# Kernel optimization log

Hardware: AMD Instinct MI355X
Metric: run time of the kernel (lower is better)

## Reference

```python
import jax, jax.numpy as jnp
import numpy as np


def setup_inputs() -> dict:
    key = jax.random.key(0)
    ks = jax.random.split(key, 4)
    B, T, C = 2, 4096, 512
    x = jax.random.normal(ks[0], (B, T, C), dtype=jnp.float32)
    Wqkv = jax.random.normal(ks[1], (C, 3 * C), dtype=jnp.float32) * (C ** -0.5)
    bqkv = jnp.zeros((3 * C,), dtype=jnp.float32)
    Wout = jax.random.normal(ks[2], (C, C), dtype=jnp.float32) * (C ** -0.5)
    bout = jnp.zeros((C,), dtype=jnp.float32)
    return {"x": x, "Wqkv": Wqkv, "bqkv": bqkv, "Wout": Wout, "bout": bout}


def reference(x, Wqkv, bqkv, Wout, bout):
    B, T, C = x.shape
    H = 8
    D = C // H  # head_dim
    qkv = x @ Wqkv + bqkv                       # [B, T, 3C]
    qkv = qkv.reshape(B, T, 3, H, D)
    q, k, v = qkv[:, :, 0], qkv[:, :, 1], qkv[:, :, 2]  # [B, T, H, D]
    scale = 1.0 / np.sqrt(D).astype(np.float32)
    scores = jnp.einsum("bqhd,bkhd->bhqk", q, k) * scale  # [B, H, T, T]
    causal = jnp.tril(jnp.ones((T, T), dtype=bool))
    scores = jnp.where(causal, scores, jnp.finfo(scores.dtype).min)
    attn = jax.nn.softmax(scores, axis=-1)                 # [B, H, T, T]
    out = jnp.einsum("bhqk,bkhd->bqhd", attn, v).reshape(B, T, C)
    return out @ Wout + bout
```

## Files before the change

kernel.cpp:

```cpp
#include <hip/hip_runtime.h>
#include <hip/hip_bf16.h>
#include <cstdint>
#include <cstddef>

typedef __attribute__((ext_vector_type(8))) __bf16 bf16x8;
typedef __attribute__((ext_vector_type(4))) float f32x4;
typedef __attribute__((ext_vector_type(16))) float f32x16;

__device__ __forceinline__ ushort f2b(float x) {
    union { float f; uint32_t u; } v; v.f = x;
    uint32_t r = v.u + 0x7FFFu + ((v.u >> 16) & 1u);
    return (ushort)(r >> 16);
}

__device__ __forceinline__ void glds16(const void* g, void* l) {
    __builtin_amdgcn_global_load_lds(
        (const __attribute__((address_space(1))) void*)g,
        (__attribute__((address_space(3))) void*)l, 16, 0, 0);
}

__device__ __forceinline__ uint32_t cvt_pk_bf16(float lo, float hi) {
    uint32_t r;
    asm("v_cvt_pk_bf16_f32 %0, %1, %2" : "=v"(r) : "v"(lo), "v"(hi));
    return r;
}

__device__ __forceinline__ void plane_swap(uint32_t& a, uint32_t& b) {
    asm volatile("v_permlane32_swap_b32 %0, %1" : "+v"(a), "+v"(b));
}

__device__ __forceinline__ f32x16 z16() {
    f32x16 v;
#pragma unroll
    for (int i = 0; i < 16; ++i) v[i] = 0.f;
    return v;
}

__global__ __launch_bounds__(256) void k_prep(const float* __restrict__ x,
                                              ushort* __restrict__ xb,
                                              const float* __restrict__ Wqkv,
                                              ushort* __restrict__ wqkvT,
                                              const float* __restrict__ Wout,
                                              ushort* __restrict__ woutT) {
    __shared__ float tile[32][33];
    const int id = blockIdx.x;
    const int tid = threadIdx.x;
    if (id < 2048) {
        const int i = id * 256 + tid;
        const float4* p = (const float4*)x + (size_t)i * 2;
        float4 a = p[0], b = p[1];
        ushort o[8] = { f2b(a.x), f2b(a.y), f2b(a.z), f2b(a.w),
                        f2b(b.x), f2b(b.y), f2b(b.z), f2b(b.w) };
        *(uint4*)(xb + (size_t)i * 8) = *(const uint4*)o;
        return;
    }
    const float* in;
    ushort* out;
    int R = 512, C, c0, r0;
    if (id < 2816) {
        in = Wqkv; out = wqkvT; C = 1536;
        c0 = ((id - 2048) % 48) * 32; r0 = ((id - 2048) / 48) * 32;
    } else {
        in = Wout; out = woutT; C = 512;
        c0 = ((id - 2816) % 16) * 32; r0 = ((id - 2816) / 16) * 32;
    }
    const int tx = tid & 31, ty = tid >> 5;
#pragma unroll
    for (int i = 0; i < 32; i += 8)
        tile[ty + i][tx] = in[(size_t)(r0 + ty + i) * C + c0 + tx];
    __syncthreads();
#pragma unroll
    for (int i = 0; i < 32; i += 8)
        out[(size_t)(c0 + ty + i) * R + r0 + tx] = f2b(tile[tx][ty + i]);
}

template <int MODE, int MP>
__global__ __launch_bounds__(256) void k_gemm(const ushort* __restrict__ A,
                                              const ushort* __restrict__ BT,
                                              const float* __restrict__ bias,
                                              float* __restrict__ outF,
                                              ushort* __restrict__ Qp,
                                              ushort* __restrict__ Kp,
                                              ushort* __restrict__ VTp,
                                              int K) {
    __shared__ __align__(16) ushort lA[2][MP * 1024];
    __shared__ __align__(16) ushort lB[2][4096];
    const int tid = threadIdx.x;
    const int lane = tid & 63, lr = lane & 15, lg = lane >> 4;
    const int wid = tid >> 6, wm = wid >> 1, wn = wid & 1;
    const int m0 = blockIdx.x * (32 * MP), n0 = blockIdx.y * 128;

    const ushort* ga = A + (size_t)(m0 + (tid >> 2)) * K + (tid & 3) * 8;
    const ushort* gb = BT + (size_t)(n0 + (tid >> 2)) * K + (tid & 3) * 8;
    const size_t rstep = (size_t)64 * K;

    float bvv[4];
#pragma unroll
    for (int n = 0; n < 4; ++n) bvv[n] = bias[n0 + wn * 64 + n * 16 + lr];
    asm volatile("s_waitcnt vmcnt(0)" ::: "memory");
    __builtin_amdgcn_sched_barrier(0);

    f32x4 zero = {0.f, 0.f, 0.f, 0.f};
    f32x4 acc[MP][4];
#pragma unroll
    for (int i = 0; i < MP; ++i)
#pragma unroll
        for (int j = 0; j < 4; ++j) acc[i][j] = zero;

    auto STG = [&](int buf, int k0) {
        glds16(ga + k0, &lA[buf][tid * 8]);
        if constexpr (MP == 4) glds16(ga + k0 + rstep, &lA[buf][2048 + tid * 8]);
        glds16(gb + k0,         &lB[buf][tid * 8]);
        glds16(gb + k0 + rstep, &lB[buf][2048 + tid * 8]);
    };

    const int NT = K >> 5;
    STG(0, 0);
    for (int it = 0; it < NT; ++it) {
        const int bsel = it & 1;
        if (it + 1 < NT) {
            STG(bsel ^ 1, (it + 1) * 32);
            if constexpr (MP == 4) {
                asm volatile("s_waitcnt vmcnt(4)" ::: "memory");
            } else {
                asm volatile("s_waitcnt vmcnt(3)" ::: "memory");
            }
        } else {
            asm volatile("s_waitcnt vmcnt(0)" ::: "memory");
        }
        __builtin_amdgcn_sched_barrier(0);
        __builtin_amdgcn_s_barrier();
        asm volatile("" ::: "memory");

        bf16x8 af[MP], bfr[4];
#pragma unroll
        for (int m = 0; m < MP; ++m)
            af[m] = *(const bf16x8*)&lA[bsel][(wm * (16 * MP) + m * 16 + lr) * 32 + lg * 8];
#pragma unroll
        for (int n = 0; n < 4; ++n)
            bfr[n] = *(const bf16x8*)&lB[bsel][(wn * 64 + n * 16 + lr) * 32 + lg * 8];
#pragma unroll
        for (int m = 0; m < MP; ++m)
#pragma unroll
            for (int n = 0; n < 4; ++n)
                acc[m][n] = __builtin_amdgcn_mfma_f32_16x16x32_bf16(af[m], bfr[n], acc[m][n], 0, 0, 0);

        asm volatile("" ::: "memory");
        __builtin_amdgcn_s_barrier();
    }

#pragma unroll
    for (int n = 0; n < 4; ++n) {
        const int gn = n0 + wn * 64 + n * 16 + lr;
        const float bv = bvv[n];
#pragma unroll
        for (int m = 0; m < MP; ++m) {
            const int gmb = m0 + wm * (16 * MP) + m * 16 + lg * 4;
            if (MODE == 0) {
                const int sec = gn >> 9, c = gn & 511;
                const int h = c >> 6, d = c & 63;
                const int b = gmb >> 12, t = gmb & 4095;
                if (sec == 2) {
                    ushort tmp[4];
#pragma unroll
                    for (int r = 0; r < 4; ++r) tmp[r] = f2b(acc[m][n][r] + bv);
                    *(ushort4*)&VTp[(size_t)(b * 8 + h) * 262144 + (size_t)d * 4096 + t] =
                        *(const ushort4*)tmp;
                } else {
                    const size_t idx0 = ((size_t)(b * 8 + h) * 4096 + t) * 64 + d;
#pragma unroll
                    for (int r = 0; r < 4; ++r) {
                        const float v = acc[m][n][r] + bv;
                        if (sec == 0) Qp[idx0 + (size_t)r * 64] = f2b(v * 0.18033688f);
                        else          Kp[idx0 + (size_t)r * 64] = f2b(v);
                    }
                }
            } else {
#pragma unroll
                for (int r = 0; r < 4; ++r)
                    outF[(size_t)(gmb + r) * 512 + gn] = acc[m][n][r] + bv;
            }
        }
    }
}

template <int MODE>
__device__ __forceinline__ void attn_run(const ushort* __restrict__ Qb,
                                         const ushort* __restrict__ Kb,
                                         const ushort* __restrict__ Vb,
                                         ushort* sm, int qt, int kv_lo, int kv_hi,
                                         int lane, int w, int tid,
                                         ushort* __restrict__ Outp, int bh,
                                         float* __restrict__ pO,
                                         float* __restrict__ pL) {
    const int lg2 = lane >> 5, l31 = lane & 31, l7 = lane & 7;
    const int q0 = qt * 256;
    const int qbase = q0 + w * 32;

    bf16x8 qf[4];
#pragma unroll
    for (int ks = 0; ks < 4; ++ks)
        qf[ks] = *(const bf16x8*)&Qb[(size_t)(qbase + l31) * 64 + ks * 16 + lg2 * 8];
    asm volatile("s_waitcnt vmcnt(0)" ::: "memory");
    __builtin_amdgcn_sched_barrier(0);

    const int srow = tid >> 3;
    const int sslot = (tid & 7) ^ (srow & 7);

    auto STAGE = [&](int buf, int kv0) {
        glds16(Kb + (size_t)(kv0 + srow) * 64 + sslot * 8,
               (char*)sm + buf * 16384 + w * 1024);
        glds16(Vb + (size_t)srow * 4096 + kv0 + sslot * 8,
               (char*)sm + buf * 16384 + 8192 + w * 1024);
    };

    f32x16 oacc0 = z16(), oacc1 = z16();
    float lrun = 0.f;

    STAGE(0, kv_lo * 64);
    for (int it = kv_lo; it < kv_hi; ++it) {
        const int kv0 = it * 64;
        const int bsel = (it - kv_lo) & 1;
        if (it + 1 < kv_hi) {
            STAGE(bsel ^ 1, kv0 + 64);
            asm volatile("s_waitcnt vmcnt(2)" ::: "memory");
        } else {
            asm volatile("s_waitcnt vmcnt(0)" ::: "memory");
        }
        __builtin_amdgcn_sched_barrier(0);
        __builtin_amdgcn_s_barrier();
        asm volatile("" ::: "memory");

        const bool live0 = (kv0 <= qbase + 31);
        const bool live1 = (kv0 + 32 <= qbase + 31);
        if (live0) {
            const ushort* bK = sm + bsel * 8192;
            const ushort* bV = bK + 4096;

            f32x16 st0 = z16(), st1 = z16();
            __builtin_amdgcn_s_setprio(1);
#pragma unroll
            for (int ks = 0; ks < 4; ++ks) {
                bf16x8 kf = *(const bf16x8*)&bK[l31 * 64 + (((2 * ks + lg2) ^ l7)) * 8];
                st0 = __builtin_amdgcn_mfma_f32_32x32x16_bf16(kf, qf[ks], st0, 0, 0, 0);
            }
            if (live1) {
#pragma unroll
                for (int ks = 0; ks < 4; ++ks) {
                    bf16x8 kf = *(const bf16x8*)&bK[(32 + l31) * 64 + (((2 * ks + lg2) ^ l7)) * 8];
                    st1 = __builtin_amdgcn_mfma_f32_32x32x16_bf16(kf, qf[ks], st1, 0, 0, 0);
                }
            }
            __builtin_amdgcn_s_setprio(0);
            if (kv0 == qbase) {
#pragma unroll
                for (int r = 0; r < 16; ++r) {
                    const int rowk = (r & 3) + 8 * (r >> 2) + 4 * lg2;
                    if (rowk > l31) st0[r] = -1e30f;
                }
            }
            if (live1 && kv0 + 32 == qbase) {
#pragma unroll
                for (int r = 0; r < 16; ++r) {
                    const int rowk = (r & 3) + 8 * (r >> 2) + 4 * lg2;
                    if (rowk > l31) st1[r] = -1e30f;
                }
            }

            float s0 = 0.f, s1 = 0.f, s2 = 0.f, s3 = 0.f;
#pragma unroll
            for (int r = 0; r < 16; r += 4) {
                st0[r]     = __builtin_amdgcn_exp2f(st0[r]);     s0 += st0[r];
                st0[r + 1] = __builtin_amdgcn_exp2f(st0[r + 1]); s1 += st0[r + 1];
                st0[r + 2] = __builtin_amdgcn_exp2f(st0[r + 2]); s2 += st0[r + 2];
                st0[r + 3] = __builtin_amdgcn_exp2f(st0[r + 3]); s3 += st0[r + 3];
            }
            if (live1) {
#pragma unroll
                for (int r = 0; r < 16; r += 4) {
                    st1[r]     = __builtin_amdgcn_exp2f(st1[r]);     s0 += st1[r];
                    st1[r + 1] = __builtin_amdgcn_exp2f(st1[r + 1]); s1 += st1[r + 1];
                    st1[r + 2] = __builtin_amdgcn_exp2f(st1[r + 2]); s2 += st1[r + 2];
                    st1[r + 3] = __builtin_amdgcn_exp2f(st1[r + 3]); s3 += st1[r + 3];
                }
            }
            lrun += (s0 + s1) + (s2 + s3);

#pragma unroll
            for (int stp = 0; stp < 4; ++stp) {
                if (stp >= 2 && !live1) continue;
                const int h = stp & 1;
                uint32_t a0, a1, b0, b1;
                if (stp < 2) {
                    a0 = cvt_pk_bf16(st0[h * 8 + 0], st0[h * 8 + 1]);
                    a1 = cvt_pk_bf16(st0[h * 8 + 2], st0[h * 8 + 3]);
                    b0 = cvt_pk_bf16(st0[h * 8 + 4], st0[h * 8 + 5]);
                    b1 = cvt_pk_bf16(st0[h * 8 + 6], st0[h * 8 + 7]);
                } else {
                    a0 = cvt_pk_bf16(st1[h * 8 + 0], st1[h * 8 + 1]);
                    a1 = cvt_pk_bf16(st1[h * 8 + 2], st1[h * 8 + 3]);
                    b0 = cvt_pk_bf16(st1[h * 8 + 4], st1[h * 8 + 5]);
                    b1 = cvt_pk_bf16(st1[h * 8 + 6], st1[h * 8 + 7]);
                }
                plane_swap(a0, b0);
                plane_swap(a1, b1);
                union { uint32_t u[4]; bf16x8 v; } pk;
                pk.u[0] = a0; pk.u[1] = a1; pk.u[2] = b0; pk.u[3] = b1;
                const int vs = (((2 * stp + lg2) ^ l7)) * 8;
                bf16x8 vf0 = *(const bf16x8*)&bV[l31 * 64 + vs];
                bf16x8 vf1 = *(const bf16x8*)&bV[(32 + l31) * 64 + vs];
                __builtin_amdgcn_s_setprio(1);
                oacc0 = __builtin_amdgcn_mfma_f32_32x32x16_bf16(vf0, pk.v, oacc0, 0, 0, 0);
                oacc1 = __builtin_amdgcn_mfma_f32_32x32x16_bf16(vf1, pk.v, oacc1, 0, 0, 0);
                __builtin_amdgcn_s_setprio(0);
            }
        }
        asm volatile("" ::: "memory");
        __builtin_amdgcn_s_barrier();
    }

    lrun += __shfl_xor(lrun, 32);

    if (MODE == 0) {
        const float inv = 1.0f / lrun;
        ushort* ep = sm + w * 2304;
#pragma unroll
        for (int r = 0; r < 16; ++r) {
            const int dd = (r & 3) + 8 * (r >> 2) + 4 * lg2;
            ep[l31 * 72 + dd]      = f2b(oacc0[r] * inv);
            ep[l31 * 72 + 32 + dd] = f2b(oacc1[r] * inv);
        }
        asm volatile("s_waitcnt lgkmcnt(0)" ::: "memory");
        __builtin_amdgcn_sched_barrier(0);
        const int qq = lane >> 1, half = lane & 1;
        const int bb = bh >> 3, hh = bh & 7;
        const int tg = q0 + w * 32 + qq;
        ushort* op = Outp + ((size_t)(bb * 4096 + tg) * 512 + hh * 64 + half * 32);
#pragma unroll
        for (int j = 0; j < 4; ++j) {
            uint4 v = *(const uint4*)&ep[qq * 72 + half * 32 + j * 8];
            *(uint4*)&op[j * 8] = v;
        }
    } else {
        const int qc = w * 32 + l31;
#pragma unroll
        for (int r = 0; r < 16; ++r) {
            const int dd = (r & 3) + 8 * (r >> 2) + 4 * lg2;
            pO[dd * 256 + qc]        = oacc0[r];
            pO[(dd + 32) * 256 + qc] = oacc1[r];
        }
        if (lg2 == 0) pL[qc] = lrun;
    }
}

__global__ __launch_bounds__(512) void k_attn(const ushort* __restrict__ Q,
                                              const ushort* __restrict__ K,
                                              const ushort* __restrict__ VT,
                                              ushort* __restrict__ Outp,
                                              float* __restrict__ pO,
                                              float* __restrict__ pL) {
    __shared__ __align__(16) ushort sm[20480];
    const int tid = threadIdx.x;
    const int lane = tid & 63, w = tid >> 6;
    const int bh = blockIdx.x;
    const int s = blockIdx.y;
    const int p = s >> 1, half = s & 1;
    const int qtH = 15 - p;
    const size_t base = (size_t)bh * 4096 * 64;
    const ushort* Qb = Q + base;
    const ushort* Kb = K + base;
    const ushort* Vb = VT + base;

    const size_t slot = (size_t)(bh * 8 + p) * 2 + half;
    if (half == 0) {
        attn_run<1>(Qb, Kb, Vb, sm, qtH, 0, 34, lane, w, tid, nullptr, bh,
                    pO + slot * 16384, pL + slot * 256);
    } else {
        attn_run<1>(Qb, Kb, Vb, sm, qtH, 34, 64 - 4 * p, lane, w, tid, nullptr, bh,
                    pO + slot * 16384, pL + slot * 256);
        attn_run<0>(Qb, Kb, Vb, sm, p, 0, 4 * p + 4, lane, w, tid, Outp, bh,
                    nullptr, nullptr);
    }
}

__global__ __launch_bounds__(512) void k_merge(const float* __restrict__ pO,
                                               const float* __restrict__ pL,
                                               ushort* __restrict__ Outp) {
    const int bh = blockIdx.x;
    const int p = blockIdx.y;
    const int tid = threadIdx.x;
    const int q = tid >> 1, dh = (tid & 1) * 32;
    const size_t slot = (size_t)(bh * 8 + p) * 2;
    const float* OA = pO + slot * 16384;
    const float* OB = OA + 16384;
    const float la = pL[slot * 256 + q];
    const float lb = pL[slot * 256 + 256 + q];
    const float inv = 1.0f / (la + lb);
    ushort outv[32];
#pragma unroll
    for (int j = 0; j < 32; ++j) {
        const float o = (OA[(dh + j) * 256 + q] + OB[(dh + j) * 256 + q]) * inv;
        outv[j] = f2b(o);
    }
    const int b = bh >> 3, h = bh & 7;
    const int t = (15 - p) * 256 + q;
    ushort* op = Outp + ((size_t)(b * 4096 + t) * 512 + h * 64 + dh);
#pragma unroll
    for (int j = 0; j < 4; ++j) *(uint4*)&op[j * 8] = *(const uint4*)&outv[j * 8];
}

extern "C" void kernel_launch(void* const* d_in, const int* in_sizes, int n_in,
                              void* d_out, int out_size, void* d_ws, size_t ws_size,
                              hipStream_t stream) {
    const float* x    = (const float*)d_in[0];
    const float* Wqkv = (const float*)d_in[1];
    const float* bqkv = (const float*)d_in[2];
    const float* Wout = (const float*)d_in[3];
    const float* bout = (const float*)d_in[4];
    float* out = (float*)d_out;

    char* ws = (char*)d_ws;
    ushort* xb    = (ushort*)(ws);
    ushort* wqkvT = (ushort*)(ws + 8388608);
    ushort* woutT = (ushort*)(ws + 9961472);
    ushort* Qp    = (ushort*)(ws + 10485760);
    ushort* Kp    = (ushort*)(ws + 18874368);
    ushort* VTp   = (ushort*)(ws + 27262976);
    float*  pO    = (float*)(ws + 35651584);
    float*  pL    = (float*)(ws + 52428800);

    k_prep<<<3072, 256, 0, stream>>>(x, xb, Wqkv, wqkvT, Wout, woutT);
    k_gemm<0, 4><<<dim3(64, 12), 256, 0, stream>>>(xb, wqkvT, bqkv, nullptr, Qp, Kp, VTp, 512);
    k_attn<<<dim3(16, 16), 512, 0, stream>>>(Qp, Kp, VTp, xb, pO, pL);
    k_merge<<<dim3(16, 8), 512, 0, stream>>>(pO, pL, xb);
    k_gemm<1, 2><<<dim3(128, 4), 256, 0, stream>>>(xb, woutT, bout, out, nullptr, nullptr, nullptr, 512);
}
```

Before: 102.8 us.

## Split attention KV ranges into finer chunks and merge bf16 partials for all tiles

The causal attention work is repartitioned. Each high/low query-tile pair is now split across four blocks of 17 KV tiles, so the grid doubles from 256 to 512 blocks and the per-block load is more even. Every block now writes unnormalized partial outputs in bf16 plus row sums. A generalized merge kernel combines 1 to 4 partials per query tile. Partial buffers are placed in reused workspace and in the output buffer. This is meant to fill the CUs better and shrink the tail of the attention kernel, at the cost of more merge traffic and extra bf16 rounding of the unnormalized partials.

Measured after the change: 97.07 us (median of 2 runs). -5.5%, faster.

```diff
diff --git a/kernel.cpp b/kernel.cpp
--- a/kernel.cpp
+++ b/kernel.cpp
@@ -11,6 +11,11 @@
     union { float f; uint32_t u; } v; v.f = x;
     uint32_t r = v.u + 0x7FFFu + ((v.u >> 16) & 1u);
     return (ushort)(r >> 16);
+}
+
+__device__ __forceinline__ float b2f(ushort u) {
+    union { uint32_t u; float f; } v; v.u = (uint32_t)u << 16;
+    return v.f;
 }
 
 __device__ __forceinline__ void glds16(const void* g, void* l) {
@@ -184,14 +189,12 @@
     }
 }
 
-template <int MODE>
 __device__ __forceinline__ void attn_run(const ushort* __restrict__ Qb,
                                          const ushort* __restrict__ Kb,
                                          const ushort* __restrict__ Vb,
                                          ushort* sm, int qt, int kv_lo, int kv_hi,
                                          int lane, int w, int tid,
-                                         ushort* __restrict__ Outp, int bh,
-                                         float* __restrict__ pO,
+                                         ushort* __restrict__ pOb,
                                          float* __restrict__ pL) {
     const int lg2 = lane >> 5, l31 = lane & 31, l7 = lane & 7;
     const int q0 = qt * 256;
@@ -320,90 +323,100 @@
     }
 
     lrun += __shfl_xor(lrun, 32);
-
-    if (MODE == 0) {
-        const float inv = 1.0f / lrun;
-        ushort* ep = sm + w * 2304;
-#pragma unroll
-        for (int r = 0; r < 16; ++r) {
-            const int dd = (r & 3) + 8 * (r >> 2) + 4 * lg2;
-            ep[l31 * 72 + dd]      = f2b(oacc0[r] * inv);
-            ep[l31 * 72 + 32 + dd] = f2b(oacc1[r] * inv);
-        }
-        asm volatile("s_waitcnt lgkmcnt(0)" ::: "memory");
-        __builtin_amdgcn_sched_barrier(0);
-        const int qq = lane >> 1, half = lane & 1;
-        const int bb = bh >> 3, hh = bh & 7;
-        const int tg = q0 + w * 32 + qq;
-        ushort* op = Outp + ((size_t)(bb * 4096 + tg) * 512 + hh * 64 + half * 32);
-#pragma unroll
-        for (int j = 0; j < 4; ++j) {
-            uint4 v = *(const uint4*)&ep[qq * 72 + half * 32 + j * 8];
-            *(uint4*)&op[j * 8] = v;
-        }
-    } else {
-        const int qc = w * 32 + l31;
-#pragma unroll
-        for (int r = 0; r < 16; ++r) {
-            const int dd = (r & 3) + 8 * (r >> 2) + 4 * lg2;
-            pO[dd * 256 + qc]        = oacc0[r];
-            pO[(dd + 32) * 256 + qc] = oacc1[r];
-        }
-        if (lg2 == 0) pL[qc] = lrun;
-    }
+    const int qc = w * 32 + l31;
+#pragma unroll
+    for (int r = 0; r < 16; ++r) {
+        const int dd = (r & 3) + 8 * (r >> 2) + 4 * lg2;
+        pOb[dd * 256 + qc]        = f2b(oacc0[r]);
+        pOb[(dd + 32) * 256 + qc] = f2b(oacc1[r]);
+    }
+    if (lg2 == 0) pL[qc] = lrun;
 }
 
 __global__ __launch_bounds__(512) void k_attn(const ushort* __restrict__ Q,
                                               const ushort* __restrict__ K,
                                               const ushort* __restrict__ VT,
-                                              ushort* __restrict__ Outp,
-                                              float* __restrict__ pO,
+                                              ushort* __restrict__ hOb,
+                                              ushort* __restrict__ lOb,
                                               float* __restrict__ pL) {
-    __shared__ __align__(16) ushort sm[20480];
+    __shared__ __align__(16) ushort sm[16384];
     const int tid = threadIdx.x;
     const int lane = tid & 63, w = tid >> 6;
     const int bh = blockIdx.x;
     const int s = blockIdx.y;
-    const int p = s >> 1, half = s & 1;
-    const int qtH = 15 - p;
+    const int p = s >> 2, half = (s >> 1) & 1, sub = s & 1;
     const size_t base = (size_t)bh * 4096 * 64;
     const ushort* Qb = Q + base;
     const ushort* Kb = K + base;
     const ushort* Vb = VT + base;
 
-    const size_t slot = (size_t)(bh * 8 + p) * 2 + half;
+    const int pairbase = bh * 8 + p;
     if (half == 0) {
-        attn_run<1>(Qb, Kb, Vb, sm, qtH, 0, 34, lane, w, tid, nullptr, bh,
-                    pO + slot * 16384, pL + slot * 256);
+        const size_t hs = (size_t)(pairbase * 4 + sub);
+        attn_run(Qb, Kb, Vb, sm, 15 - p, 17 * sub, 17 * sub + 17, lane, w, tid,
+                 hOb + hs * 16384, pL + hs * 256);
     } else {
-        attn_run<1>(Qb, Kb, Vb, sm, qtH, 34, 64 - 4 * p, lane, w, tid, nullptr, bh,
-                    pO + slot * 16384, pL + slot * 256);
-        attn_run<0>(Qb, Kb, Vb, sm, p, 0, 4 * p + 4, lane, w, tid, Outp, bh,
-                    nullptr, nullptr);
-    }
-}
-
-__global__ __launch_bounds__(512) void k_merge(const float* __restrict__ pO,
+        const int nH2 = 30 - 4 * p;
+        if (17 * sub < nH2) {
+            const int hi = 17 * sub + 17 < nH2 ? 17 * sub + 17 : nH2;
+            const size_t hs = (size_t)(pairbase * 4 + 2 + sub);
+            attn_run(Qb, Kb, Vb, sm, 15 - p, 34 + 17 * sub, 34 + hi, lane, w, tid,
+                     hOb + hs * 16384, pL + hs * 256);
+        }
+        if (17 * sub + 17 > nH2) {
+            const int nL = 4 * p + 4;
+            int llo = 17 * sub - nH2; if (llo < 0) llo = 0;
+            int lhi = 17 * sub + 17 - nH2; if (lhi > nL) lhi = nL;
+            const int lidx = (p <= 3) ? 0 : sub;
+            const size_t ls = (size_t)(pairbase * 2 + lidx);
+            attn_run(Qb, Kb, Vb, sm, p, llo, lhi, lane, w, tid,
+                     lOb + ls * 16384, pL + (size_t)(512 + ls) * 256);
+        }
+    }
+}
+
+__global__ __launch_bounds__(512) void k_merge(const ushort* __restrict__ hOb,
+                                               const ushort* __restrict__ lOb,
                                                const float* __restrict__ pL,
                                                ushort* __restrict__ Outp) {
     const int bh = blockIdx.x;
-    const int p = blockIdx.y;
+    const int qt = blockIdx.y;
     const int tid = threadIdx.x;
     const int q = tid >> 1, dh = (tid & 1) * 32;
-    const size_t slot = (size_t)(bh * 8 + p) * 2;
-    const float* OA = pO + slot * 16384;
-    const float* OB = OA + 16384;
-    const float la = pL[slot * 256 + q];
-    const float lb = pL[slot * 256 + 256 + q];
-    const float inv = 1.0f / (la + lb);
+
+    int k;
+    const ushort* Ob;
+    const float* Lb;
+    if (qt >= 8) {
+        const int p = 15 - qt;
+        k = (p <= 3) ? 4 : 3;
+        const size_t s0 = (size_t)((bh * 8 + p) * 4);
+        Ob = hOb + s0 * 16384;
+        Lb = pL + s0 * 256;
+    } else {
+        const int p = qt;
+        k = (p <= 3) ? 1 : 2;
+        const size_t s0 = (size_t)((bh * 8 + p) * 2);
+        Ob = lOb + s0 * 16384;
+        Lb = pL + (size_t)(512 + s0) * 256;
+    }
+
+    float osum[32];
+#pragma unroll
+    for (int e = 0; e < 32; ++e) osum[e] = 0.f;
+    float lsum = 0.f;
+    for (int j = 0; j < k; ++j) {
+        const ushort* O = Ob + (size_t)j * 16384;
+#pragma unroll
+        for (int e = 0; e < 32; ++e) osum[e] += b2f(O[(dh + e) * 256 + q]);
+        lsum += Lb[(size_t)j * 256 + q];
+    }
+    const float inv = 1.0f / lsum;
     ushort outv[32];
 #pragma unroll
-    for (int j = 0; j < 32; ++j) {
-        const float o = (OA[(dh + j) * 256 + q] + OB[(dh + j) * 256 + q]) * inv;
-        outv[j] = f2b(o);
-    }
+    for (int e = 0; e < 32; ++e) outv[e] = f2b(osum[e] * inv);
     const int b = bh >> 3, h = bh & 7;
-    const int t = (15 - p) * 256 + q;
+    const int t = qt * 256 + q;
     ushort* op = Outp + ((size_t)(b * 4096 + t) * 512 + h * 64 + dh);
 #pragma unroll
     for (int j = 0; j < 4; ++j) *(uint4*)&op[j * 8] = *(const uint4*)&outv[j * 8];
@@ -426,12 +439,13 @@
     ushort* Qp    = (ushort*)(ws + 10485760);
     ushort* Kp    = (ushort*)(ws + 18874368);
     ushort* VTp   = (ushort*)(ws + 27262976);
-    float*  pO    = (float*)(ws + 35651584);
-    float*  pL    = (float*)(ws + 52428800);
+    ushort* hOb   = (ushort*)(ws + 35651584);
+    ushort* lOb   = (ushort*)d_out;
+    float*  pL    = (float*)(ws + 8388608);
 
     k_prep<<<3072, 256, 0, stream>>>(x, xb, Wqkv, wqkvT, Wout, woutT);
     k_gemm<0, 4><<<dim3(64, 12), 256, 0, stream>>>(xb, wqkvT, bqkv, nullptr, Qp, Kp, VTp, 512);
-    k_attn<<<dim3(16, 16), 512, 0, stream>>>(Qp, Kp, VTp, xb, pO, pL);
-    k_merge<<<dim3(16, 8), 512, 0, stream>>>(pO, pL, xb);
+    k_attn<<<dim3(16, 32), 512, 0, stream>>>(Qp, Kp, VTp, hOb, lOb, pL);
+    k_merge<<<dim3(16, 16), 512, 0, stream>>>(hOb, lOb, pL, xb);
     k_gemm<1, 2><<<dim3(128, 4), 256, 0, stream>>>(xb, woutT, bout, out, nullptr, nullptr, nullptr, 512);
 }
```
